# Performance work log

Hardware: AMD Instinct MI355X
Metric: run time of the kernel (lower is better)

The kernel has to match this reference:

```python
import jax, jax.numpy as jnp
import numpy as np

DIM, R, HEAD = 512, 4, 8
HD = DIM // HEAD
SCALE = HD ** -0.5
EPS = 1e-5


def dwconv(x, w, b, stride, padding):
    # depthwise conv (groups == channels) + bias + relu; x:[B,C,H,W], w:[C,1,kh,kw]
    y = jax.lax.conv_general_dilated(
        x, w, window_strides=stride, padding=padding,
        feature_group_count=x.shape[1],
        dimension_numbers=('NCHW', 'OIHW', 'NCHW'))
    return jax.nn.relu(y + b[None, :, None, None])


def setup_inputs() -> dict:
    key = jax.random.key(0)
    ks = jax.random.split(key, 12)
    s = 0.02
    return {
        'x': jax.random.normal(ks[0], (8, DIM, 56, 56), dtype=jnp.float32),
        'Wq': jax.random.normal(ks[1], (DIM, DIM), dtype=jnp.float32) * s,
        'bq': jnp.zeros((DIM,), jnp.float32),
        'Wkv': jax.random.normal(ks[2], (2 * DIM, DIM), dtype=jnp.float32) * s,
        'bkv': jnp.zeros((2 * DIM,), jnp.float32),
        'w1a': jax.random.normal(ks[3], (DIM, 1, 1, R), dtype=jnp.float32) * s,
        'b1a': jnp.zeros((DIM,), jnp.float32),
        'w1b': jax.random.normal(ks[4], (DIM, 1, R, 1), dtype=jnp.float32) * s,
        'b1b': jnp.zeros((DIM,), jnp.float32),
        'w2': jax.random.normal(ks[5], (DIM, 1, R, R), dtype=jnp.float32) * s,
        'b2': jnp.zeros((DIM,), jnp.float32),
        'w3': jax.random.normal(ks[6], (DIM, 1, 3, 3), dtype=jnp.float32) * s,
        'b3': jnp.zeros((DIM,), jnp.float32),
        'gamma': jnp.ones((DIM,), jnp.float32),
        'beta': jnp.zeros((DIM,), jnp.float32),
    }


def reference(x, Wq, bq, Wkv, bkv, w1a, b1a, w1b, b1b, w2, b2, w3, b3, gamma, beta):
    B, C, H, W = x.shape
    N = H * W
    x_layer = x.reshape(B, C, N).transpose(0, 2, 1)  # [B,N,C]
    q = (x_layer @ Wq.T + bq).reshape(B, N, HEAD, HD).transpose(0, 2, 1, 3)  # [B,h,N,d]

    # branch 1: (1,R)s(1,R) dwconv -> (R,1)s(R,1) dwconv
    l1 = dwconv(dwconv(x, w1a, b1a, (1, R), ((0, 0), (0, 0))),
                w1b, b1b, (R, 1), ((0, 0), (0, 0))).reshape(B, C, -1)
    # branch 2: RxR stride-R dwconv
    l2 = dwconv(x, w2, b2, (R, R), ((0, 0), (0, 0))).reshape(B, C, -1)
    # branch 3: avg-pool to (H/R, W/R) then 3x3 dwconv pad 1
    l3 = x.reshape(B, C, H // R, R, W // R, R).mean(axis=(3, 5))
    l3 = dwconv(l3, w3, b3, (1, 1), ((1, 1), (1, 1))).reshape(B, C, -1)

    l_ = jnp.concatenate([l1, l2, l3], axis=2).transpose(0, 2, 1)  # [B,M,C]
    mu = l_.mean(-1, keepdims=True)
    var = ((l_ - mu) ** 2).mean(-1, keepdims=True)
    l_ = (l_ - mu) * jax.lax.rsqrt(var + EPS) * gamma + beta

    M = l_.shape[1]
    kv = (l_ @ Wkv.T + bkv).reshape(B, M, 2, HEAD, HD).transpose(2, 0, 3, 1, 4)
    k, v = kv[0], kv[1]  # [B,h,M,d]

    attn = jax.nn.softmax(jnp.einsum('bhid,bhjd->bhij', q, k) * SCALE, axis=-1)
    out = jnp.einsum('bhij,bhjd->bhid', attn, v).transpose(0, 2, 1, 3).reshape(B, N, C)
    # NOTE: original torch code computes proj(out) but then overwrites it with
    # proj_drop(out); with drop=0 the returned value is exactly `out`.
    return out
```

## Files before the change

### kernel.cpp

```cpp
#include <hip/hip_runtime.h>
#include <hip/hip_bf16.h>

#define BATCH   8
#define C_DIM   512
#define HWD     56
#define NPIX    3136
#define PW      14
#define PP      196
#define M_TOT   588
#define BM_ROWS 4704
#define BM_PAD  4736
#define HEADS   8
#define HD      64
#define N_SEQ   3136
#define SM_SCALE 0.125f
#define SM_SCALE_LOG2E 0.1803368801111204f

#define KS_STRIDE 68
#define KS_ROWS   592
#define VS_STRIDE 596
#define ATTN_LDS_SHORTS (KS_ROWS * KS_STRIDE + 64 * VS_STRIDE)
#define ATTN_LDS_BYTES  (ATTN_LDS_SHORTS * 2)

typedef __attribute__((ext_vector_type(8))) short bf16x8;
typedef __attribute__((ext_vector_type(4))) short bf16x4;
typedef __attribute__((ext_vector_type(4))) float f32x4;

__device__ __forceinline__ short f2bs(float f) {
    __hip_bfloat16 h = __float2bfloat16(f);
    return *reinterpret_cast<short*>(&h);
}
__device__ __forceinline__ unsigned pkbf(float lo, float hi) {
    __hip_bfloat162 t = __float22bfloat162_rn(make_float2(lo, hi));
    return *reinterpret_cast<unsigned*>(&t);
}
__device__ __forceinline__ float fexp2(float x) {
#if __has_builtin(__builtin_amdgcn_exp2f)
    return __builtin_amdgcn_exp2f(x);
#else
    return exp2f(x);
#endif
}

__device__ __forceinline__ f32x4 mfma16(bf16x4 a, bf16x4 b, f32x4 c) {
#if __has_builtin(__builtin_amdgcn_mfma_f32_16x16x16bf16_1k)
    return __builtin_amdgcn_mfma_f32_16x16x16bf16_1k(a, b, c, 0, 0, 0);
#elif __has_builtin(__builtin_amdgcn_mfma_f32_16x16x16_bf16)
    return __builtin_amdgcn_mfma_f32_16x16x16_bf16(a, b, c, 0, 0, 0);
#else
    asm volatile("v_mfma_f32_16x16x16_bf16 %0, %1, %2, %0\n\ts_nop 7\n\ts_nop 1"
                 : "+v"(c) : "v"(a), "v"(b));
    return c;
#endif
}

__device__ __forceinline__ void gl_lds16(const void* g, void* l) {
    __builtin_amdgcn_global_load_lds(
        (const __attribute__((address_space(1))) void*)g,
        (__attribute__((address_space(3))) void*)l, 16, 0, 0);
}

__global__ __launch_bounds__(256) void k_branches(
    const float* __restrict__ x,
    const float* __restrict__ w1a, const float* __restrict__ b1a,
    const float* __restrict__ w1b, const float* __restrict__ b1b,
    const float* __restrict__ w2,  const float* __restrict__ b2,
    const float* __restrict__ w3,  const float* __restrict__ b3,
    float* __restrict__ l_pre)
{
    __shared__ float xs[NPIX];
    __shared__ float y1s[HWD * PW];
    __shared__ float pools[PP];
    const int c = blockIdx.x, b = blockIdx.y, tid = threadIdx.x;
    const float* xp = x + ((size_t)(b * C_DIM + c)) * NPIX;
    for (int i = tid; i < NPIX / 4; i += 256)
        ((float4*)xs)[i] = ((const float4*)xp)[i];
    __syncthreads();

    const float wa0 = w1a[c*4+0], wa1 = w1a[c*4+1], wa2 = w1a[c*4+2], wa3 = w1a[c*4+3];
    const float ba = b1a[c];
    for (int i = tid; i < HWD * PW; i += 256) {
        int h = i / PW, w = i % PW;
        const float* r = xs + h * HWD + w * 4;
        float v = ba + r[0]*wa0 + r[1]*wa1 + r[2]*wa2 + r[3]*wa3;
        y1s[i] = fmaxf(v, 0.f);
    }
    if (tid < PP) {
        int h = tid / PW, w = tid % PW;
        float s = 0.f;
        #pragma unroll
        for (int r = 0; r < 4; ++r) {
            const float* rr = xs + (h*4 + r) * HWD + w * 4;
            s += rr[0] + rr[1] + rr[2] + rr[3];
        }
        pools[tid] = s * (1.f / 16.f);
    }
    __syncthreads();

    if (tid < PP) {
        int h = tid / PW, w = tid % PW;
        float* lp = l_pre + ((size_t)(b * C_DIM + c)) * M_TOT;
        float v1 = b1b[c];
        v1 += y1s[(h*4+0)*PW + w] * w1b[c*4+0];
        v1 += y1s[(h*4+1)*PW + w] * w1b[c*4+1];
        v1 += y1s[(h*4+2)*PW + w] * w1b[c*4+2];
        v1 += y1s[(h*4+3)*PW + w] * w1b[c*4+3];
        lp[tid] = fmaxf(v1, 0.f);
        float v2 = b2[c];
        #pragma unroll
        for (int r = 0; r < 4; ++r)
            #pragma unroll
            for (int s2 = 0; s2 < 4; ++s2)
                v2 += xs[(h*4+r)*HWD + w*4 + s2] * w2[c*16 + r*4 + s2];
        lp[PP + tid] = fmaxf(v2, 0.f);
        float v3 = b3[c];
        #pragma unroll
        for (int dh = -1; dh <= 1; ++dh)
            #pragma unroll
            for (int dw = -1; dw <= 1; ++dw) {
                int hh = h + dh, ww = w + dw;
                if (hh >= 0 && hh < PW && ww >= 0 && ww < PW)
                    v3 += pools[hh*PW + ww] * w3[c*9 + (dh+1)*3 + (dw+1)];
            }
        lp[2*PP + tid] = fmaxf(v3, 0.f);
    }
}

__global__ __launch_bounds__(256) void k_stats(
    const float* __restrict__ l_pre, float2* __restrict__ stats)
{
    __shared__ float ssum[4][64];
    __shared__ float ssq[4][64];
    const int tid = threadIdx.x;
    const int ml = tid & 63, cg = tid >> 6;
    const int b = blockIdx.y;
    const int m = blockIdx.x * 64 + ml;
    float s = 0.f, q = 0.f;
    if (m < M_TOT) {
        const float* base = l_pre + ((size_t)b * C_DIM + cg * 128) * M_TOT + m;
        for (int c = 0; c < 128; ++c) {
            float v = base[(size_t)c * M_TOT];
            s += v; q += v * v;
        }
    }
    ssum[cg][ml] = s; ssq[cg][ml] = q;
    __syncthreads();
    if (tid < 64 && blockIdx.x * 64 + tid < M_TOT) {
        float ts = ssum[0][tid] + ssum[1][tid] + ssum[2][tid] + ssum[3][tid];
        float tq = ssq[0][tid] + ssq[1][tid] + ssq[2][tid] + ssq[3][tid];
        float mu = ts * (1.f / 512.f);
        float var = tq * (1.f / 512.f) - mu * mu;
        stats[(size_t)b * M_TOT + blockIdx.x * 64 + tid] =
            make_float2(mu, rsqrtf(var + 1e-5f));
    }
}

__global__ __launch_bounds__(256) void k_wconv(
    const float* __restrict__ Wq, const float* __restrict__ Wkv,
    short* __restrict__ Wqb, short* __restrict__ Wkvb)
{
    int i = (blockIdx.x * 256 + threadIdx.x) * 4;
    if (i < 262144) {
        float4 v = *(const float4*)(Wq + i);
        short o[4] = {f2bs(v.x), f2bs(v.y), f2bs(v.z), f2bs(v.w)};
        *(short4*)(Wqb + i) = *(short4*)o;
    } else {
        int j = i - 262144;
        float4 v = *(const float4*)(Wkv + j);
        short o[4] = {f2bs(v.x), f2bs(v.y), f2bs(v.z), f2bs(v.w)};
        *(short4*)(Wkvb + j) = *(short4*)o;
    }
}

__global__ __launch_bounds__(256) void k_xpose(
    const float* __restrict__ x, short* __restrict__ Xb)
{
    __shared__ float sx[64][68];
    const int tid = threadIdx.x;
    const int n0 = blockIdx.x * 64, c0 = blockIdx.y * 64, b = blockIdx.z;
    #pragma unroll
    for (int it = 0; it < 4; ++it) {
        int idx = tid + it * 256;
        int cr = idx >> 4, n4 = (idx & 15) * 4;
        float4 v = *(const float4*)(x + ((size_t)(b * C_DIM + c0 + cr)) * NPIX + n0 + n4);
        *(float4*)&sx[cr][n4] = v;
    }
    __syncthreads();
    #pragma unroll
    for (int p = 0; p < 2; ++p) {
        int idx = tid + p * 256;
        int nr = idx >> 3, cg = (idx & 7) * 8;
        short ov[8];
        #pragma unroll
        for (int e = 0; e < 8; ++e) ov[e] = f2bs(sx[cg + e][nr]);
        *(float4*)&Xb[((size_t)(b * NPIX + n0 + nr)) * C_DIM + c0 + cg] = *(float4*)ov;
    }
}

__global__ __launch_bounds__(256) void k_lnt(
    const float* __restrict__ l_pre, const float2* __restrict__ stats,
    const float* __restrict__ gamma, const float* __restrict__ beta,
    short* __restrict__ Lb)
{
    __shared__ float sx[64][68];
    const int tid = threadIdx.x;
    const int m0 = blockIdx.x * 64, c0 = blockIdx.y * 64, b = blockIdx.z;
    #pragma unroll
    for (int it = 0; it < 4; ++it) {
        int idx = tid + it * 256;
        int cr = idx >> 4, m4 = (idx & 15) * 4;
        float4 v = {0.f, 0.f, 0.f, 0.f};
        if (m0 + m4 < M_TOT)
            v = *(const float4*)(l_pre + ((size_t)(b * C_DIM + c0 + cr)) * M_TOT + m0 + m4);
        *(float4*)&sx[cr][m4] = v;
    }
    __syncthreads();
    #pragma unroll
    for (int p = 0; p < 2; ++p) {
        int idx = tid + p * 256;
        int mr = idx >> 3, cg = (idx & 7) * 8;
        int m = m0 + mr;
        float mu = 0.f, rstd = 0.f;
        if (m < M_TOT) {
            float2 st = stats[(size_t)b * M_TOT + m];
            mu = st.x; rstd = st.y;
        }
        short ov[8];
        #pragma unroll
        for (int e = 0; e < 8; ++e) {
            int c = c0 + cg + e;
            ov[e] = f2bs((sx[cg + e][mr] - mu) * rstd * gamma[c] + beta[c]);
        }
        if (m < M_TOT)
            *(float4*)&Lb[((size_t)(b * M_TOT + m)) * C_DIM + c0 + cg] = *(float4*)ov;
    }
}

__global__ __launch_bounds__(256) void k_gemm_q(
    const short* __restrict__ A, const short* __restrict__ Bw,
    const float* __restrict__ bias, short* __restrict__ Qb)
{
    __shared__ short As[128 * 64];
    __shared__ short Bs[128 * 64];
    const int tid = threadIdx.x;
    const int lane = tid & 63, w = tid >> 6;
    const int l15 = lane & 15, quad = lane >> 4;
    const int wr = w & 1, wc = w >> 1;
    const int row0 = blockIdx.x * 128, col0 = blockIdx.y * 128;
    const int lr8 = lane >> 3, lc8 = (lane & 7) * 8;

    f32x4 acc[4][4] = {};

    for (int c0 = 0; c0 < 512; c0 += 64) {
        __syncthreads();
        #pragma unroll
        for (int it = 0; it < 4; ++it) {
            int r = w * 32 + it * 8;
            gl_lds16(A  + (size_t)(row0 + r + lr8) * 512 + c0 + lc8, &As[r * 64]);
            gl_lds16(Bw + (size_t)(col0 + r + lr8) * 512 + c0 + lc8, &Bs[r * 64]);
        }
        __syncthreads();
        #pragma unroll
        for (int ks = 0; ks < 2; ++ks) {
            bf16x8 af[4], bf[4];
            #pragma unroll
            for (int t = 0; t < 4; ++t) {
                af[t] = *(const bf16x8*)&As[(wr*64 + t*16 + l15)*64 + ks*32 + quad*8];
                bf[t] = *(const bf16x8*)&Bs[(wc*64 + t*16 + l15)*64 + ks*32 + quad*8];
            }
            #pragma unroll
            for (int nt = 0; nt < 4; ++nt)
                #pragma unroll
                for (int mt = 0; mt < 4; ++mt)
                    acc[nt][mt] = __builtin_amdgcn_mfma_f32_16x16x32_bf16(
                        af[nt], bf[mt], acc[nt][mt], 0, 0, 0);
        }
    }

    #pragma unroll
    for (int nt = 0; nt < 4; ++nt) {
        int row_t = row0 + wr * 64 + nt * 16 + quad * 4;
        #pragma unroll
        for (int mt = 0; mt < 4; ++mt) {
            int col = col0 + wc * 64 + mt * 16 + l15;
            float bv = bias[col];
            int h = col >> 6, d = col & 63;
            #pragma unroll
            for (int r = 0; r < 4; ++r) {
                int row_g = row_t + r;
                int b = row_g / N_SEQ;
                int n = row_g - b * N_SEQ;
                Qb[(((size_t)(b * HEADS + h)) * N_SEQ + n) * HD + d] =
                    f2bs((acc[nt][mt][r] + bv) * SM_SCALE_LOG2E);
            }
        }
    }
}

__global__ __launch_bounds__(256) void k_gemm_kv(
    const short* __restrict__ A, const short* __restrict__ Bw,
    const float* __restrict__ bias,
    short* __restrict__ Kb, short* __restrict__ Vt)
{
    __shared__ short As[128 * 64];
    __shared__ short Bs[128 * 64];
    const int tid = threadIdx.x;
    const int lane = tid & 63, w = tid >> 6;
    const int l15 = lane & 15, quad = lane >> 4;
    const int wr = w & 1, wc = w >> 1;
    const int row0 = blockIdx.x * 128, col0 = blockIdx.y * 128;
    const int lr8 = lane >> 3, lc8 = (lane & 7) * 8;

    f32x4 acc[4][4] = {};

    for (int c0 = 0; c0 < 512; c0 += 64) {
        __syncthreads();
        #pragma unroll
        for (int it = 0; it < 4; ++it) {
            int r = w * 32 + it * 8;
            gl_lds16(A  + (size_t)(row0 + r + lr8) * 512 + c0 + lc8, &As[r * 64]);
            gl_lds16(Bw + (size_t)(col0 + r + lr8) * 512 + c0 + lc8, &Bs[r * 64]);
        }
        __syncthreads();
        #pragma unroll
        for (int ks = 0; ks < 2; ++ks) {
            bf16x8 af[4], bf[4];
            #pragma unroll
            for (int t = 0; t < 4; ++t) {
                af[t] = *(const bf16x8*)&As[(wr*64 + t*16 + l15)*64 + ks*32 + quad*8];
                bf[t] = *(const bf16x8*)&Bs[(wc*64 + t*16 + l15)*64 + ks*32 + quad*8];
            }
            #pragma unroll
            for (int nt = 0; nt < 4; ++nt)
                #pragma unroll
                for (int mt = 0; mt < 4; ++mt)
                    acc[nt][mt] = __builtin_amdgcn_mfma_f32_16x16x32_bf16(
                        af[nt], bf[mt], acc[nt][mt], 0, 0, 0);
        }
    }

    #pragma unroll
    for (int nt = 0; nt < 4; ++nt) {
        int row_t = row0 + wr * 64 + nt * 16 + quad * 4;
        #pragma unroll
        for (int mt = 0; mt < 4; ++mt) {
            int col = col0 + wc * 64 + mt * 16 + l15;
            float bv = bias[col];
            #pragma unroll
            for (int r = 0; r < 4; ++r) {
                int row_g = row_t + r;
                float v = acc[nt][mt][r] + bv;
                if (row_g < BM_ROWS) {
                    int b = row_g / M_TOT;
                    int m = row_g - b * M_TOT;
                    if (col < 512) {
                        int h = col >> 6, d = col & 63;
                        Kb[(((size_t)(b * HEADS + h)) * M_TOT + m) * HD + d] = f2bs(v);
                    } else {
                        int jj = col - 512, h = jj >> 6, d = jj & 63;
                        Vt[(((size_t)(b * HEADS + h)) * HD + d) * M_TOT + m] = f2bs(v);
                    }
                }
            }
        }
    }
}

__global__ __launch_bounds__(1024) void k_attn(
    const short* __restrict__ Qb, const short* __restrict__ Kb,
    const short* __restrict__ Vt, float* __restrict__ out)
{
    extern __shared__ short smem[];
    short* Ks = smem;
    short* Vs = smem + KS_ROWS * KS_STRIDE;

    const int tid = threadIdx.x;
    const int lane = tid & 63, w = tid >> 6;
    const int l15 = lane & 15, quad = lane >> 4;
    const int q4 = blockIdx.x, h = blockIdx.y, b = blockIdx.z;
    const size_t bh = (size_t)(b * HEADS + h);
    const size_t kbase = bh * M_TOT * HD;
    const size_t vbase = bh * (size_t)HD * M_TOT;

    for (int i = tid; i < 4704; i += 1024) {
        int row = i >> 3, seg = i & 7;
        *(float4*)&Ks[row * KS_STRIDE + seg * 8] =
            *(const float4*)(Kb + kbase + (size_t)row * 64 + seg * 8);
    }
    if (tid < 256) {
        int r = tid >> 6, cc = tid & 63;
        Ks[(588 + r) * KS_STRIDE + cc] = 0;
    }
    {
        int row = tid >> 4, tg = tid & 15;
        const short* src = Vt + vbase + (size_t)row * M_TOT;
        #pragma unroll 2
        for (int jj = tg; jj < 147; jj += 16)
            *(float2*)&Vs[row * VS_STRIDE + jj * 4] = *(const float2*)(src + jj * 4);
    }
    if (tid < 512) {
        int row = tid >> 3, cc = tid & 7;
        Vs[row * VS_STRIDE + 588 + cc] = 0;
    }
    __syncthreads();

    const bf16x4 ones = {(short)0x3F80, (short)0x3F80, (short)0x3F80, (short)0x3F80};

    for (int ds = w; ds < 25; ds += 16) {
        const bool sbv = (ds < 24);
        const int nA = q4 * 784 + ds * 32 + l15;
        const int nB = sbv ? nA + 16 : nA;

        bf16x8 qfA[2], qfB[2];
        #pragma unroll
        for (int ks = 0; ks < 2; ++ks) {
            qfA[ks] = *(const bf16x8*)(Qb + (bh * N_SEQ + nA) * HD + ks * 32 + quad * 8);
            qfB[ks] = *(const bf16x8*)(Qb + (bh * N_SEQ + nB) * HD + ks * 32 + quad * 8);
        }

        f32x4 oaccA[4] = {}, oaccB[4] = {};
        f32x4 rsaccA = {}, rsaccB = {};

        auto LOAD = [&](int j0, bf16x8& K0, bf16x8& K1,
                        bf16x4& V0, bf16x4& V1, bf16x4& V2, bf16x4& V3) {
            const short* kr = &Ks[(j0 + l15) * KS_STRIDE + quad * 8];
            K0 = *(const bf16x8*)kr;
            K1 = *(const bf16x8*)(kr + 32);
            const short* vr = &Vs[l15 * VS_STRIDE + j0 + quad * 4];
            V0 = *(const bf16x4*)vr;
            V1 = *(const bf16x4*)(vr + 16 * VS_STRIDE);
            V2 = *(const bf16x4*)(vr + 32 * VS_STRIDE);
            V3 = *(const bf16x4*)(vr + 48 * VS_STRIDE);
        };

        auto STEP = [&](bf16x8 K0, bf16x8 K1,
                        bf16x4 V0, bf16x4 V1, bf16x4 V2, bf16x4 V3) {
            f32x4 sA = {}, sB = {};
            sA = __builtin_amdgcn_mfma_f32_16x16x32_bf16(K0, qfA[0], sA, 0, 0, 0);
            sB = __builtin_amdgcn_mfma_f32_16x16x32_bf16(K0, qfB[0], sB, 0, 0, 0);
            sA = __builtin_amdgcn_mfma_f32_16x16x32_bf16(K1, qfA[1], sA, 0, 0, 0);
            sB = __builtin_amdgcn_mfma_f32_16x16x32_bf16(K1, qfB[1], sB, 0, 0, 0);

            float pA[4], pB[4];
            #pragma unroll
            for (int r = 0; r < 4; ++r) {
                pA[r] = fexp2(sA[r]);
                pB[r] = fexp2(sB[r]);
            }
            unsigned ua[2] = {pkbf(pA[0], pA[1]), pkbf(pA[2], pA[3])};
            unsigned ub[2] = {pkbf(pB[0], pB[1]), pkbf(pB[2], pB[3])};
            bf16x4 pbA, pbB;
            __builtin_memcpy(&pbA, ua, 8);
            __builtin_memcpy(&pbB, ub, 8);

            rsaccA = mfma16(ones, pbA, rsaccA);
            rsaccB = mfma16(ones, pbB, rsaccB);

            oaccA[0] = mfma16(V0, pbA, oaccA[0]);
            oaccB[0] = mfma16(V0, pbB, oaccB[0]);
            oaccA[1] = mfma16(V1, pbA, oaccA[1]);
            oaccB[1] = mfma16(V1, pbB, oaccB[1]);
            oaccA[2] = mfma16(V2, pbA, oaccA[2]);
            oaccB[2] = mfma16(V2, pbB, oaccB[2]);
            oaccA[3] = mfma16(V3, pbA, oaccA[3]);
            oaccB[3] = mfma16(V3, pbB, oaccB[3]);
        };

        bf16x8 k0a, k1a, k0b, k1b;
        bf16x4 v0a, v1a, v2a, v3a, v0b, v1b, v2b, v3b;

        LOAD(0, k0a, k1a, v0a, v1a, v2a, v3a);
        __builtin_amdgcn_sched_barrier(0);
        #pragma unroll 1
        for (int t = 0; t < 18; ++t) {
            const int j0 = t * 32;
            LOAD(j0 + 16, k0b, k1b, v0b, v1b, v2b, v3b);
            __builtin_amdgcn_sched_barrier(0);
            STEP(k0a, k1a, v0a, v1a, v2a, v3a);
            LOAD(j0 + 32, k0a, k1a, v0a, v1a, v2a, v3a);
            __builtin_amdgcn_sched_barrier(0);
            STEP(k0b, k1b, v0b, v1b, v2b, v3b);
        }
        STEP(k0a, k1a, v0a, v1a, v2a, v3a);

        const float invA = 1.f / (rsaccA[0] - 4.f);
        const float invB = 1.f / (rsaccB[0] - 4.f);
        float* orowA = out + ((size_t)b * N_SEQ + nA) * C_DIM + h * HD;
        #pragma unroll
        for (int dt = 0; dt < 4; ++dt) {
            float4 o;
            o.x = oaccA[dt][0] * invA; o.y = oaccA[dt][1] * invA;
            o.z = oaccA[dt][2] * invA; o.w = oaccA[dt][3] * invA;
            *(float4*)&orowA[dt * 16 + quad * 4] = o;
        }
        if (sbv) {
            float* orowB = out + ((size_t)b * N_SEQ + nB) * C_DIM + h * HD;
            #pragma unroll
            for (int dt = 0; dt < 4; ++dt) {
                float4 o;
                o.x = oaccB[dt][0] * invB; o.y = oaccB[dt][1] * invB;
                o.z = oaccB[dt][2] * invB; o.w = oaccB[dt][3] * invB;
                *(float4*)&orowB[dt * 16 + quad * 4] = o;
            }
        }
    }
}

extern "C" void kernel_launch(void* const* d_in, const int* in_sizes, int n_in,
                              void* d_out, int out_size, void* d_ws, size_t ws_size,
                              hipStream_t stream) {
    const float* x     = (const float*)d_in[0];
    const float* Wq    = (const float*)d_in[1];
    const float* bq    = (const float*)d_in[2];
    const float* Wkv   = (const float*)d_in[3];
    const float* bkv   = (const float*)d_in[4];
    const float* w1a   = (const float*)d_in[5];
    const float* b1a   = (const float*)d_in[6];
    const float* w1b   = (const float*)d_in[7];
    const float* b1b   = (const float*)d_in[8];
    const float* w2    = (const float*)d_in[9];
    const float* b2    = (const float*)d_in[10];
    const float* w3    = (const float*)d_in[11];
    const float* b3    = (const float*)d_in[12];
    const float* gamma = (const float*)d_in[13];
    const float* beta  = (const float*)d_in[14];
    float* out = (float*)d_out;

    char* ws = (char*)d_ws;
    short*  Xb    = (short*)ws;
    float*  l_pre = (float*)ws;
    float2* stats = (float2*)(ws + 9633792);
    short*  Lb    = (short*)(ws + 9671424);
    short*  Wqb   = (short*)(ws + 25690112);
    short*  Wkvb  = (short*)(ws + 26214400);
    short*  Kb    = (short*)(ws + 27262976);
    short*  Vt    = (short*)(ws + 32079872);
    short*  Qb    = (short*)(ws + 36896768);

    static bool attr_set = false;
    hipFuncSetAttribute((const void*)k_attn,
                        hipFuncAttributeMaxDynamicSharedMemorySize,
                        ATTN_LDS_BYTES);
    (void)attr_set;

    k_wconv<<<768, 256, 0, stream>>>(Wq, Wkv, Wqb, Wkvb);
    k_xpose<<<dim3(49, 8, BATCH), 256, 0, stream>>>(x, Xb);
    k_gemm_q<<<dim3(196, 4), 256, 0, stream>>>(Xb, Wqb, bq, Qb);
    k_branches<<<dim3(C_DIM, BATCH), 256, 0, stream>>>(
        x, w1a, b1a, w1b, b1b, w2, b2, w3, b3, l_pre);
    k_stats<<<dim3(10, BATCH), 256, 0, stream>>>(l_pre, stats);
    k_lnt<<<dim3(10, 8, BATCH), 256, 0, stream>>>(l_pre, stats, gamma, beta, Lb);
    k_gemm_kv<<<dim3(37, 8), 256, 0, stream>>>(Lb, Wkvb, bkv, Kb, Vt);
    k_attn<<<dim3(4, HEADS, BATCH), 1024, ATTN_LDS_BYTES, stream>>>(Qb, Kb, Vt, out);
}
```

Measured before the change: 274.9 us.

## Merge independent front-end kernels into combined launches and prioritize attention MFMA

Folds the weight-conversion, transpose and branch-conv kernels into one heterogeneous launch (k_front), and the Q GEMM plus LayerNorm statistics into a second (k_mid). Both dispatch on block index, which cuts the number of launches and lets independent work share the GPU at the same time. Workspace buffers are remapped, with stats and Lb placed in the output buffer, so the concurrent stages do not overwrite each other. The attention inner loop also raises wave priority around its MFMA groups with s_setprio. The shared LDS size now fits the larger body, which may reduce occupancy for the smaller tasks.

```diff
diff --git a/kernel.cpp b/kernel.cpp
--- a/kernel.cpp
+++ b/kernel.cpp
@@ -60,7 +60,9 @@
         (__attribute__((address_space(3))) void*)l, 16, 0, 0);
 }
 
-__global__ __launch_bounds__(256) void k_branches(
+
+__device__ __forceinline__ void branches_body(
+    int c, int b, int tid, float* sbuf,
     const float* __restrict__ x,
     const float* __restrict__ w1a, const float* __restrict__ b1a,
     const float* __restrict__ w1b, const float* __restrict__ b1b,
@@ -68,10 +70,9 @@
     const float* __restrict__ w3,  const float* __restrict__ b3,
     float* __restrict__ l_pre)
 {
-    __shared__ float xs[NPIX];
-    __shared__ float y1s[HWD * PW];
-    __shared__ float pools[PP];
-    const int c = blockIdx.x, b = blockIdx.y, tid = threadIdx.x;
+    float* xs    = sbuf;
+    float* y1s   = sbuf + 3136;
+    float* pools = sbuf + 3920;
     const float* xp = x + ((size_t)(b * C_DIM + c)) * NPIX;
     for (int i = tid; i < NPIX / 4; i += 256)
         ((float4*)xs)[i] = ((const float4*)xp)[i];
@@ -126,40 +127,37 @@
     }
 }
 
-__global__ __launch_bounds__(256) void k_stats(
-    const float* __restrict__ l_pre, float2* __restrict__ stats)
-{
-    __shared__ float ssum[4][64];
-    __shared__ float ssq[4][64];
-    const int tid = threadIdx.x;
-    const int ml = tid & 63, cg = tid >> 6;
-    const int b = blockIdx.y;
-    const int m = blockIdx.x * 64 + ml;
-    float s = 0.f, q = 0.f;
-    if (m < M_TOT) {
-        const float* base = l_pre + ((size_t)b * C_DIM + cg * 128) * M_TOT + m;
-        for (int c = 0; c < 128; ++c) {
-            float v = base[(size_t)c * M_TOT];
-            s += v; q += v * v;
-        }
-    }
-    ssum[cg][ml] = s; ssq[cg][ml] = q;
+__device__ __forceinline__ void xpose_body(
+    int bx, int by, int bz, int tid, float* sbuf,
+    const float* __restrict__ x, short* __restrict__ Xb)
+{
+    float (*sx)[68] = (float(*)[68])sbuf;
+    const int n0 = bx * 64, c0 = by * 64, b = bz;
+    #pragma unroll
+    for (int it = 0; it < 4; ++it) {
+        int idx = tid + it * 256;
+        int cr = idx >> 4, n4 = (idx & 15) * 4;
+        float4 v = *(const float4*)(x + ((size_t)(b * C_DIM + c0 + cr)) * NPIX + n0 + n4);
+        *(float4*)&sx[cr][n4] = v;
+    }
     __syncthreads();
-    if (tid < 64 && blockIdx.x * 64 + tid < M_TOT) {
-        float ts = ssum[0][tid] + ssum[1][tid] + ssum[2][tid] + ssum[3][tid];
-        float tq = ssq[0][tid] + ssq[1][tid] + ssq[2][tid] + ssq[3][tid];
-        float mu = ts * (1.f / 512.f);
-        float var = tq * (1.f / 512.f) - mu * mu;
-        stats[(size_t)b * M_TOT + blockIdx.x * 64 + tid] =
-            make_float2(mu, rsqrtf(var + 1e-5f));
-    }
-}
-
-__global__ __launch_bounds__(256) void k_wconv(
+    #pragma unroll
+    for (int p = 0; p < 2; ++p) {
+        int idx = tid + p * 256;
+        int nr = idx >> 3, cg = (idx & 7) * 8;
+        short ov[8];
+        #pragma unroll
+        for (int e = 0; e < 8; ++e) ov[e] = f2bs(sx[cg + e][nr]);
+        *(float4*)&Xb[((size_t)(b * NPIX + n0 + nr)) * C_DIM + c0 + cg] = *(float4*)ov;
+    }
+}
+
+__device__ __forceinline__ void wconv_body(
+    int blk, int tid,
     const float* __restrict__ Wq, const float* __restrict__ Wkv,
     short* __restrict__ Wqb, short* __restrict__ Wkvb)
 {
-    int i = (blockIdx.x * 256 + threadIdx.x) * 4;
+    int i = (blk * 256 + tid) * 4;
     if (i < 262144) {
         float4 v = *(const float4*)(Wq + i);
         short o[4] = {f2bs(v.x), f2bs(v.y), f2bs(v.z), f2bs(v.w)};
@@ -172,28 +170,132 @@
     }
 }
 
-__global__ __launch_bounds__(256) void k_xpose(
-    const float* __restrict__ x, short* __restrict__ Xb)
-{
-    __shared__ float sx[64][68];
-    const int tid = threadIdx.x;
-    const int n0 = blockIdx.x * 64, c0 = blockIdx.y * 64, b = blockIdx.z;
+__global__ __launch_bounds__(256) void k_front(
+    const float* __restrict__ x,
+    const float* __restrict__ Wq, const float* __restrict__ Wkv,
+    short* __restrict__ Wqb, short* __restrict__ Wkvb,
+    short* __restrict__ Xb,
+    const float* __restrict__ w1a, const float* __restrict__ b1a,
+    const float* __restrict__ w1b, const float* __restrict__ b1b,
+    const float* __restrict__ w2,  const float* __restrict__ b2,
+    const float* __restrict__ w3,  const float* __restrict__ b3,
+    float* __restrict__ l_pre)
+{
+    __shared__ float sbuf[4368];
+    const int bid = blockIdx.x, tid = threadIdx.x;
+    if (bid < 4096) {
+        branches_body(bid & 511, bid >> 9, tid, sbuf,
+                      x, w1a, b1a, w1b, b1b, w2, b2, w3, b3, l_pre);
+    } else if (bid < 7232) {
+        int i2 = bid - 4096;
+        xpose_body(i2 % 49, (i2 / 49) & 7, i2 / 392, tid, sbuf, x, Xb);
+    } else {
+        wconv_body(bid - 7232, tid, Wq, Wkv, Wqb, Wkvb);
+    }
+}
+
+
+__device__ __forceinline__ void gemm_q_body(
+    int bx, int by, int tid, short* As, short* Bs,
+    const short* __restrict__ A, const short* __restrict__ Bw,
+    const float* __restrict__ bias, short* __restrict__ Qb)
+{
+    const int lane = tid & 63, w = tid >> 6;
+    const int l15 = lane & 15, quad = lane >> 4;
+    const int wr = w & 1, wc = w >> 1;
+    const int row0 = bx * 128, col0 = by * 128;
+    const int lr8 = lane >> 3, lc8 = (lane & 7) * 8;
+
+    f32x4 acc[4][4] = {};
+
+    for (int c0 = 0; c0 < 512; c0 += 64) {
+        __syncthreads();
+        #pragma unroll
+        for (int it = 0; it < 4; ++it) {
+            int r = w * 32 + it * 8;
+            gl_lds16(A  + (size_t)(row0 + r + lr8) * 512 + c0 + lc8, &As[r * 64]);
+            gl_lds16(Bw + (size_t)(col0 + r + lr8) * 512 + c0 + lc8, &Bs[r * 64]);
+        }
+        __syncthreads();
+        #pragma unroll
+        for (int ks = 0; ks < 2; ++ks) {
+            bf16x8 af[4], bf[4];
+            #pragma unroll
+            for (int t = 0; t < 4; ++t) {
+                af[t] = *(const bf16x8*)&As[(wr*64 + t*16 + l15)*64 + ks*32 + quad*8];
+                bf[t] = *(const bf16x8*)&Bs[(wc*64 + t*16 + l15)*64 + ks*32 + quad*8];
+            }
+            #pragma unroll
+            for (int nt = 0; nt < 4; ++nt)
+                #pragma unroll
+                for (int mt = 0; mt < 4; ++mt)
+                    acc[nt][mt] = __builtin_amdgcn_mfma_f32_16x16x32_bf16(
+                        af[nt], bf[mt], acc[nt][mt], 0, 0, 0);
+        }
+    }
+
     #pragma unroll
-    for (int it = 0; it < 4; ++it) {
-        int idx = tid + it * 256;
-        int cr = idx >> 4, n4 = (idx & 15) * 4;
-        float4 v = *(const float4*)(x + ((size_t)(b * C_DIM + c0 + cr)) * NPIX + n0 + n4);
-        *(float4*)&sx[cr][n4] = v;
-    }
+    for (int nt = 0; nt < 4; ++nt) {
+        int row_t = row0 + wr * 64 + nt * 16 + quad * 4;
+        #pragma unroll
+        for (int mt = 0; mt < 4; ++mt) {
+            int col = col0 + wc * 64 + mt * 16 + l15;
+            float bv = bias[col];
+            int h = col >> 6, d = col & 63;
+            #pragma unroll
+            for (int r = 0; r < 4; ++r) {
+                int row_g = row_t + r;
+                int b = row_g / N_SEQ;
+                int n = row_g - b * N_SEQ;
+                Qb[(((size_t)(b * HEADS + h)) * N_SEQ + n) * HD + d] =
+                    f2bs((acc[nt][mt][r] + bv) * SM_SCALE_LOG2E);
+            }
+        }
+    }
+}
+
+__device__ __forceinline__ void stats_body(
+    int sx_, int sb_, int tid, float* red,
+    const float* __restrict__ l_pre, float2* __restrict__ stats)
+{
+    float* ssum = red;
+    float* ssq  = red + 256;
+    const int ml = tid & 63, cg = tid >> 6;
+    const int b = sb_;
+    const int m = sx_ * 64 + ml;
+    float s = 0.f, q = 0.f;
+    if (m < M_TOT) {
+        const float* base = l_pre + ((size_t)b * C_DIM + cg * 128) * M_TOT + m;
+        for (int c = 0; c < 128; ++c) {
+            float v = base[(size_t)c * M_TOT];
+            s += v; q += v * v;
+        }
+    }
+    ssum[cg*64 + ml] = s; ssq[cg*64 + ml] = q;
     __syncthreads();
-    #pragma unroll
-    for (int p = 0; p < 2; ++p) {
-        int idx = tid + p * 256;
-        int nr = idx >> 3, cg = (idx & 7) * 8;
-        short ov[8];
-        #pragma unroll
-        for (int e = 0; e < 8; ++e) ov[e] = f2bs(sx[cg + e][nr]);
-        *(float4*)&Xb[((size_t)(b * NPIX + n0 + nr)) * C_DIM + c0 + cg] = *(float4*)ov;
+    if (tid < 64 && sx_ * 64 + tid < M_TOT) {
+        float ts = ssum[tid] + ssum[64+tid] + ssum[128+tid] + ssum[192+tid];
+        float tq = ssq[tid] + ssq[64+tid] + ssq[128+tid] + ssq[192+tid];
+        float mu = ts * (1.f / 512.f);
+        float var = tq * (1.f / 512.f) - mu * mu;
+        stats[(size_t)b * M_TOT + sx_ * 64 + tid] =
+            make_float2(mu, rsqrtf(var + 1e-5f));
+    }
+}
+
+__global__ __launch_bounds__(256) void k_mid(
+    const short* __restrict__ Xb, const short* __restrict__ Wqb,
+    const float* __restrict__ bq, short* __restrict__ Qb,
+    const float* __restrict__ l_pre, float2* __restrict__ stats)
+{
+    __shared__ short sb2[16384];
+    const int bid = blockIdx.x, tid = threadIdx.x;
+    if (bid < 784) {
+        gemm_q_body(bid % 196, bid / 196, tid, sb2, sb2 + 8192,
+                    Xb, Wqb, bq, Qb);
+    } else {
+        int sid = bid - 784;
+        stats_body(sid % 10, sid / 10, tid, (float*)sb2, l_pre, stats);
     }
 }
 
@@ -233,67 +335,6 @@
         }
         if (m < M_TOT)
             *(float4*)&Lb[((size_t)(b * M_TOT + m)) * C_DIM + c0 + cg] = *(float4*)ov;
-    }
-}
-
-__global__ __launch_bounds__(256) void k_gemm_q(
-    const short* __restrict__ A, const short* __restrict__ Bw,
-    const float* __restrict__ bias, short* __restrict__ Qb)
-{
-    __shared__ short As[128 * 64];
-    __shared__ short Bs[128 * 64];
-    const int tid = threadIdx.x;
-    const int lane = tid & 63, w = tid >> 6;
-    const int l15 = lane & 15, quad = lane >> 4;
-    const int wr = w & 1, wc = w >> 1;
-    const int row0 = blockIdx.x * 128, col0 = blockIdx.y * 128;
-    const int lr8 = lane >> 3, lc8 = (lane & 7) * 8;
-
-    f32x4 acc[4][4] = {};
-
-    for (int c0 = 0; c0 < 512; c0 += 64) {
-        __syncthreads();
-        #pragma unroll
-        for (int it = 0; it < 4; ++it) {
-            int r = w * 32 + it * 8;
-            gl_lds16(A  + (size_t)(row0 + r + lr8) * 512 + c0 + lc8, &As[r * 64]);
-            gl_lds16(Bw + (size_t)(col0 + r + lr8) * 512 + c0 + lc8, &Bs[r * 64]);
-        }
-        __syncthreads();
-        #pragma unroll
-        for (int ks = 0; ks < 2; ++ks) {
-            bf16x8 af[4], bf[4];
-            #pragma unroll
-            for (int t = 0; t < 4; ++t) {
-                af[t] = *(const bf16x8*)&As[(wr*64 + t*16 + l15)*64 + ks*32 + quad*8];
-                bf[t] = *(const bf16x8*)&Bs[(wc*64 + t*16 + l15)*64 + ks*32 + quad*8];
-            }
-            #pragma unroll
-            for (int nt = 0; nt < 4; ++nt)
-                #pragma unroll
-                for (int mt = 0; mt < 4; ++mt)
-                    acc[nt][mt] = __builtin_amdgcn_mfma_f32_16x16x32_bf16(
-                        af[nt], bf[mt], acc[nt][mt], 0, 0, 0);
-        }
-    }
-
-    #pragma unroll
-    for (int nt = 0; nt < 4; ++nt) {
-        int row_t = row0 + wr * 64 + nt * 16 + quad * 4;
-        #pragma unroll
-        for (int mt = 0; mt < 4; ++mt) {
-            int col = col0 + wc * 64 + mt * 16 + l15;
-            float bv = bias[col];
-            int h = col >> 6, d = col & 63;
-            #pragma unroll
-            for (int r = 0; r < 4; ++r) {
-                int row_g = row_t + r;
-                int b = row_g / N_SEQ;
-                int n = row_g - b * N_SEQ;
-                Qb[(((size_t)(b * HEADS + h)) * N_SEQ + n) * HD + d] =
-                    f2bs((acc[nt][mt][r] + bv) * SM_SCALE_LOG2E);
-            }
-        }
     }
 }
 
@@ -436,10 +477,12 @@
         auto STEP = [&](bf16x8 K0, bf16x8 K1,
                         bf16x4 V0, bf16x4 V1, bf16x4 V2, bf16x4 V3) {
             f32x4 sA = {}, sB = {};
+            __builtin_amdgcn_s_setprio(1);
             sA = __builtin_amdgcn_mfma_f32_16x16x32_bf16(K0, qfA[0], sA, 0, 0, 0);
             sB = __builtin_amdgcn_mfma_f32_16x16x32_bf16(K0, qfB[0], sB, 0, 0, 0);
             sA = __builtin_amdgcn_mfma_f32_16x16x32_bf16(K1, qfA[1], sA, 0, 0, 0);
             sB = __builtin_amdgcn_mfma_f32_16x16x32_bf16(K1, qfB[1], sB, 0, 0, 0);
+            __builtin_amdgcn_s_setprio(0);
 
             float pA[4], pB[4];
             #pragma unroll
@@ -453,6 +496,7 @@
             __builtin_memcpy(&pbA, ua, 8);
             __builtin_memcpy(&pbB, ub, 8);
 
+            __builtin_amdgcn_s_setprio(1);
             rsaccA = mfma16(ones, pbA, rsaccA);
             rsaccB = mfma16(ones, pbB, rsaccB);
 
@@ -464,6 +508,7 @@
             oaccB[2] = mfma16(V2, pbB, oaccB[2]);
             oaccA[3] = mfma16(V3, pbA, oaccA[3]);
             oaccB[3] = mfma16(V3, pbB, oaccB[3]);
+            __builtin_amdgcn_s_setprio(0);
         };
 
         bf16x8 k0a, k1a, k0b, k1b;
@@ -528,27 +573,23 @@
 
     char* ws = (char*)d_ws;
     short*  Xb    = (short*)ws;
-    float*  l_pre = (float*)ws;
-    float2* stats = (float2*)(ws + 9633792);
-    short*  Lb    = (short*)(ws + 9671424);
     short*  Wqb   = (short*)(ws + 25690112);
     short*  Wkvb  = (short*)(ws + 26214400);
+    float*  l_pre = (float*)(ws + 27262976);
     short*  Kb    = (short*)(ws + 27262976);
     short*  Vt    = (short*)(ws + 32079872);
     short*  Qb    = (short*)(ws + 36896768);
-
-    static bool attr_set = false;
+    float2* stats = (float2*)d_out;
+    short*  Lb    = (short*)((char*)d_out + 65536);
+
     hipFuncSetAttribute((const void*)k_attn,
                         hipFuncAttributeMaxDynamicSharedMemorySize,
                         ATTN_LDS_BYTES);
-    (void)attr_set;
-
-    k_wconv<<<768, 256, 0, stream>>>(Wq, Wkv, Wqb, Wkvb);
-    k_xpose<<<dim3(49, 8, BATCH), 256, 0, stream>>>(x, Xb);
-    k_gemm_q<<<dim3(196, 4), 256, 0, stream>>>(Xb, Wqb, bq, Qb);
-    k_branches<<<dim3(C_DIM, BATCH), 256, 0, stream>>>(
-        x, w1a, b1a, w1b, b1b, w2, b2, w3, b3, l_pre);
-    k_stats<<<dim3(10, BATCH), 256, 0, stream>>>(l_pre, stats);
+
+    k_front<<<8000, 256, 0, stream>>>(
+        x, Wq, Wkv, Wqb, Wkvb, Xb,
+        w1a, b1a, w1b, b1b, w2, b2, w3, b3, l_pre);
+    k_mid<<<864, 256, 0, stream>>>(Xb, Wqb, bq, Qb, l_pre, stats);
     k_lnt<<<dim3(10, 8, BATCH), 256, 0, stream>>>(l_pre, stats, gamma, beta, Lb);
     k_gemm_kv<<<dim3(37, 8), 256, 0, stream>>>(Lb, Wkvb, bkv, Kb, Vt);
     k_attn<<<dim3(4, HEADS, BATCH), 1024, ATTN_LDS_BYTES, stream>>>(Qb, Kb, Vt, out);
```

Result: faster. 257.3 us, median of 2 (-6.4%).
